# Performance work log

Hardware: AMD Instinct MI355X
Metric: run time of the kernel (lower is better)

## Reference

```python
import jax, jax.numpy as jnp
import numpy as np

N_NODES = 100000


def gcn_conv(x, W, b, src, dst, deg_inv_sqrt):
    # x: [N, Cin], W: [Cin, Cout]. PyG GCNConv: transform then normalized aggregate.
    h = x @ W  # [N, Cout]
    norm = deg_inv_sqrt[src] * deg_inv_sqrt[dst]  # [E']
    msg = h[src] * norm[:, None]  # gather + scale
    out = jax.ops.segment_sum(msg, dst, num_segments=N_NODES)
    return out + b


def setup_inputs() -> dict:
    key = jax.random.key(0)
    ks = jax.random.split(key, 8)
    C = 256
    E = 3200000
    x = jax.random.normal(ks[0], (N_NODES, C), dtype=jnp.float32)
    edge_index = jax.random.randint(ks[1], (2, E), 0, N_NODES, dtype=jnp.int64)
    s = 1.0 / np.sqrt(C)
    W1 = jax.random.uniform(ks[2], (C, C), jnp.float32, -s, s)
    b1 = jnp.zeros((C,), jnp.float32)
    W2 = jax.random.uniform(ks[3], (C, C), jnp.float32, -s, s)
    b2 = jnp.zeros((C,), jnp.float32)
    Wl = jax.random.uniform(ks[4], (C, 1), jnp.float32, -s, s)
    bl = jnp.zeros((1,), jnp.float32)
    return {"x": x, "edge_index": edge_index, "W1": W1, "b1": b1,
            "W2": W2, "b2": b2, "Wl": Wl, "bl": bl}


def reference(x, edge_index, W1, b1, W2, b2, Wl, bl):
    # add self-loops once (shared by both conv layers)
    loops = jnp.arange(N_NODES, dtype=edge_index.dtype)
    src = jnp.concatenate([edge_index[0], loops])
    dst = jnp.concatenate([edge_index[1], loops])
    # symmetric normalization: deg counts incoming edges incl. self-loops
    deg = jax.ops.segment_sum(jnp.ones_like(dst, dtype=x.dtype), dst,
                              num_segments=N_NODES)
    deg_inv_sqrt = jax.lax.rsqrt(deg)  # deg >= 1 due to self-loops
    h = jax.nn.relu(gcn_conv(x, W1, b1, src, dst, deg_inv_sqrt))
    h = jax.nn.relu(gcn_conv(h, W2, b2, src, dst, deg_inv_sqrt))
    return h @ Wl + bl  # [N, 1]
```

## Files before the change

kernel.cpp:

```cpp
#include <hip/hip_runtime.h>

#define NN 100000
#define CC 256
#define EE 3200000

typedef __attribute__((ext_vector_type(8))) short bf16x8;
typedef __attribute__((ext_vector_type(4))) float f32x4;
typedef __attribute__((ext_vector_type(4))) _Float16 f16x4;

__device__ __forceinline__ float4 f4add(float4 a, float4 b) {
  return make_float4(a.x + b.x, a.y + b.y, a.z + b.z, a.w + b.w);
}

__device__ __forceinline__ unsigned short f2bf(float f) {
  unsigned u = __float_as_uint(f);
  unsigned r = (u + 0x7fffu + ((u >> 16) & 1u)) >> 16;
  return (unsigned short)r;
}
__device__ __forceinline__ float bf2f(unsigned short h) {
  return __uint_as_float(((unsigned)h) << 16);
}

__global__ void k_deg(const int* __restrict__ dst, int* __restrict__ cnt, int n) {
  int i = blockIdx.x * blockDim.x + threadIdx.x;
  int stride = gridDim.x * blockDim.x;
  for (; i < n; i += stride) {
    unsigned d = (unsigned)dst[i];
    if (d < NN) atomicAdd(&cnt[d], 1);
  }
}

__global__ void k_dis(const int* __restrict__ cnt, float* __restrict__ dis, int n) {
  int i = blockIdx.x * blockDim.x + threadIdx.x;
  if (i < n) dis[i] = 1.0f / sqrtf((float)(cnt[i] + 1));
}

__global__ void k_scan_local(const int* __restrict__ cnt, int* __restrict__ offs,
                             int* __restrict__ bsum, int n) {
  __shared__ int wsum[16];
  int t = threadIdx.x;
  int idx = blockIdx.x * 1024 + t;
  int lane = t & 63, wv = t >> 6;
  int v = (idx < n) ? cnt[idx] : 0;
  int x = v;
#pragma unroll
  for (int d = 1; d < 64; d <<= 1) {
    int y = __shfl_up(x, d, 64);
    if (lane >= d) x += y;
  }
  if (lane == 63) wsum[wv] = x;
  __syncthreads();
  int wpre = 0, total = 0;
#pragma unroll
  for (int w = 0; w < 16; ++w) {
    int s = wsum[w];
    if (w < wv) wpre += s;
    total += s;
  }
  if (idx < n) offs[idx] = wpre + x - v;
  if (t == 0) bsum[blockIdx.x] = total;
}

__global__ void k_scan_bsum(const int* __restrict__ bsum, int* __restrict__ bbase, int nb) {
  __shared__ int wsum[2];
  int t = threadIdx.x;
  int lane = t & 63, wv = t >> 6;
  int v = (t < nb) ? bsum[t] : 0;
  int x = v;
#pragma unroll
  for (int d = 1; d < 64; d <<= 1) {
    int y = __shfl_up(x, d, 64);
    if (lane >= d) x += y;
  }
  if (lane == 63) wsum[wv] = x;
  __syncthreads();
  int pre = (wv == 1) ? wsum[0] : 0;
  if (t < nb) bbase[t] = pre + x - v;
  if (t == nb - 1) bbase[nb] = pre + x;
}

__global__ void k_scan_add(int* __restrict__ offs, const int* __restrict__ bbase,
                           int n, int nb) {
  int i = blockIdx.x * 256 + threadIdx.x;
  if (i < n) offs[i] += bbase[i >> 10];
  if (i == 0) offs[n] = bbase[nb];
}

__global__ void k_scatter(const int* __restrict__ src, const int* __restrict__ dst,
                          const int* __restrict__ offs, int* __restrict__ fill,
                          int* __restrict__ csr, int n) {
  int i = blockIdx.x * blockDim.x + threadIdx.x;
  int stride = gridDim.x * blockDim.x;
  for (; i < n; i += stride) {
    unsigned d = (unsigned)dst[i];
    unsigned s = (unsigned)src[i];
    if (d < NN && s < NN) {
      int p = offs[d] + atomicAdd(&fill[d], 1);
      csr[p] = (int)s;
    }
  }
}

__global__ void k_wsplit(const float* __restrict__ W, unsigned short* __restrict__ WTh,
                         unsigned short* __restrict__ WTl) {
  int k = blockIdx.x, n = threadIdx.x;
  float w = W[k * CC + n];
  unsigned short h = f2bf(w);
  unsigned short l = f2bf(w - bf2f(h));
  WTh[n * CC + k] = h;
  WTl[n * CC + k] = l;
}

#define LDA 40

__global__ __launch_bounds__(256) void k_gemm_mfma(
    const float* __restrict__ A, const unsigned short* __restrict__ WTh,
    const unsigned short* __restrict__ WTl, const float* __restrict__ dis,
    _Float16* __restrict__ Out, int M) {
  __shared__ unsigned short Ah[128 * LDA], Al[128 * LDA];
  __shared__ unsigned short Bh[128 * LDA], Bl[128 * LDA];
  const int tid = threadIdx.x;
  const int wave = tid >> 6, lane = tid & 63;
  const int quad = lane >> 4, l16 = lane & 15;
  const int wm = wave >> 1, wn = wave & 1;
  const int row0 = blockIdx.x * 128;
  const int n0 = blockIdx.y * 128;

  f32x4 acc[4][4];
#pragma unroll
  for (int i = 0; i < 4; ++i)
#pragma unroll
    for (int j = 0; j < 4; ++j) acc[i][j] = (f32x4){0.f, 0.f, 0.f, 0.f};

  for (int k0 = 0; k0 < CC; k0 += 32) {
#pragma unroll
    for (int q = 0; q < 4; ++q) {
      int idx = tid + 256 * q;
      int r = idx >> 3;
      int c4 = (idx & 7) << 2;
      int gr = row0 + r;
      float4 v = make_float4(0.f, 0.f, 0.f, 0.f);
      if (gr < M) v = *(const float4*)&A[(size_t)gr * CC + k0 + c4];
      ushort4 hv, lv;
      hv.x = f2bf(v.x); lv.x = f2bf(v.x - bf2f(hv.x));
      hv.y = f2bf(v.y); lv.y = f2bf(v.y - bf2f(hv.y));
      hv.z = f2bf(v.z); lv.z = f2bf(v.z - bf2f(hv.z));
      hv.w = f2bf(v.w); lv.w = f2bf(v.w - bf2f(hv.w));
      *(ushort4*)&Ah[r * LDA + c4] = hv;
      *(ushort4*)&Al[r * LDA + c4] = lv;
    }
#pragma unroll
    for (int q = 0; q < 4; ++q) {
      int idx = tid + 256 * q;
      int r = idx >> 3;
      int c4 = (idx & 7) << 2;
      const size_t g = (size_t)(n0 + r) * CC + k0 + c4;
      *(ushort4*)&Bh[r * LDA + c4] = *(const ushort4*)&WTh[g];
      *(ushort4*)&Bl[r * LDA + c4] = *(const ushort4*)&WTl[g];
    }
    __syncthreads();

    bf16x8 bh[4], bl[4];
#pragma unroll
    for (int j = 0; j < 4; ++j) {
      int br = (wn * 64 + j * 16 + l16) * LDA + quad * 8;
      bh[j] = *(const bf16x8*)&Bh[br];
      bl[j] = *(const bf16x8*)&Bl[br];
    }
#pragma unroll
    for (int i = 0; i < 4; ++i) {
      int ar = (wm * 64 + i * 16 + l16) * LDA + quad * 8;
      bf16x8 ah = *(const bf16x8*)&Ah[ar];
      bf16x8 al = *(const bf16x8*)&Al[ar];
#pragma unroll
      for (int j = 0; j < 4; ++j) {
        acc[i][j] = __builtin_amdgcn_mfma_f32_16x16x32_bf16(ah, bh[j], acc[i][j], 0, 0, 0);
        acc[i][j] = __builtin_amdgcn_mfma_f32_16x16x32_bf16(al, bh[j], acc[i][j], 0, 0, 0);
        acc[i][j] = __builtin_amdgcn_mfma_f32_16x16x32_bf16(ah, bl[j], acc[i][j], 0, 0, 0);
      }
    }
    __syncthreads();
  }

#pragma unroll
  for (int i = 0; i < 4; ++i) {
#pragma unroll
    for (int r4 = 0; r4 < 4; ++r4) {
      int r = row0 + wm * 64 + i * 16 + quad * 4 + r4;
      if (r < M) {
        float sc = dis[r];
#pragma unroll
        for (int j = 0; j < 4; ++j) {
          Out[(size_t)r * CC + n0 + wn * 64 + j * 16 + l16] =
              (_Float16)(acc[i][j][r4] * sc);
        }
      }
    }
  }
}

__global__ __launch_bounds__(256) void k_aggregate(
    const _Float16* __restrict__ hs, const int* __restrict__ offs,
    const int* __restrict__ csr, const float* __restrict__ dis,
    const float* __restrict__ bias, float* __restrict__ out, int n) {
  int node = blockIdx.x * 4 + (threadIdx.x >> 6);
  if (node >= n) return;
  int lane = threadIdx.x & 63;
  int c4 = lane << 2;
  int beg = offs[node], end = offs[node + 1];
  f16x4 sv = *(const f16x4*)&hs[(size_t)node * CC + c4];
  float4 a0 = make_float4((float)sv.x, (float)sv.y, (float)sv.z, (float)sv.w);
  float4 a1 = make_float4(0.f, 0.f, 0.f, 0.f);
  int e = beg;
  for (; e + 2 <= end; e += 2) {
    int s0 = csr[e], s1 = csr[e + 1];
    f16x4 v0 = *(const f16x4*)&hs[(size_t)s0 * CC + c4];
    f16x4 v1 = *(const f16x4*)&hs[(size_t)s1 * CC + c4];
    a0.x += (float)v0.x; a0.y += (float)v0.y; a0.z += (float)v0.z; a0.w += (float)v0.w;
    a1.x += (float)v1.x; a1.y += (float)v1.y; a1.z += (float)v1.z; a1.w += (float)v1.w;
  }
  if (e < end) {
    int s0 = csr[e];
    f16x4 v0 = *(const f16x4*)&hs[(size_t)s0 * CC + c4];
    a0.x += (float)v0.x; a0.y += (float)v0.y; a0.z += (float)v0.z; a0.w += (float)v0.w;
  }
  float4 acc = f4add(a0, a1);
  float sc = dis[node];
  float4 bv = *(const float4*)&bias[c4];
  float4 r;
  r.x = fmaxf(acc.x * sc + bv.x, 0.f);
  r.y = fmaxf(acc.y * sc + bv.y, 0.f);
  r.z = fmaxf(acc.z * sc + bv.z, 0.f);
  r.w = fmaxf(acc.w * sc + bv.w, 0.f);
  *(float4*)&out[(size_t)node * CC + c4] = r;
}

__global__ __launch_bounds__(256) void k_aggregate_final(
    const _Float16* __restrict__ hs, const int* __restrict__ offs,
    const int* __restrict__ csr, const float* __restrict__ dis,
    const float* __restrict__ bias, const float* __restrict__ Wl,
    const float* __restrict__ bl, float* __restrict__ out, int n) {
  int node = blockIdx.x * 4 + (threadIdx.x >> 6);
  if (node >= n) return;
  int lane = threadIdx.x & 63;
  int c4 = lane << 2;
  int beg = offs[node], end = offs[node + 1];
  f16x4 sv = *(const f16x4*)&hs[(size_t)node * CC + c4];
  float4 a0 = make_float4((float)sv.x, (float)sv.y, (float)sv.z, (float)sv.w);
  float4 a1 = make_float4(0.f, 0.f, 0.f, 0.f);
  int e = beg;
  for (; e + 2 <= end; e += 2) {
    int s0 = csr[e], s1 = csr[e + 1];
    f16x4 v0 = *(const f16x4*)&hs[(size_t)s0 * CC + c4];
    f16x4 v1 = *(const f16x4*)&hs[(size_t)s1 * CC + c4];
    a0.x += (float)v0.x; a0.y += (float)v0.y; a0.z += (float)v0.z; a0.w += (float)v0.w;
    a1.x += (float)v1.x; a1.y += (float)v1.y; a1.z += (float)v1.z; a1.w += (float)v1.w;
  }
  if (e < end) {
    int s0 = csr[e];
    f16x4 v0 = *(const f16x4*)&hs[(size_t)s0 * CC + c4];
    a0.x += (float)v0.x; a0.y += (float)v0.y; a0.z += (float)v0.z; a0.w += (float)v0.w;
  }
  float4 acc = f4add(a0, a1);
  float sc = dis[node];
  float4 bv = *(const float4*)&bias[c4];
  float4 w = *(const float4*)&Wl[c4];
  float s = fmaxf(acc.x * sc + bv.x, 0.f) * w.x +
            fmaxf(acc.y * sc + bv.y, 0.f) * w.y +
            fmaxf(acc.z * sc + bv.z, 0.f) * w.z +
            fmaxf(acc.w * sc + bv.w, 0.f) * w.w;
#pragma unroll
  for (int d = 32; d > 0; d >>= 1) s += __shfl_down(s, d, 64);
  if (lane == 0) out[node] = s + bl[0];
}

extern "C" void kernel_launch(void* const* d_in, const int* in_sizes, int n_in,
                              void* d_out, int out_size, void* d_ws, size_t ws_size,
                              hipStream_t stream) {
  const float* x = (const float*)d_in[0];
  const int* ei = (const int*)d_in[1];
  const float* W1 = (const float*)d_in[2];
  const float* b1 = (const float*)d_in[3];
  const float* W2 = (const float*)d_in[4];
  const float* b2 = (const float*)d_in[5];
  const float* Wl = (const float*)d_in[6];
  const float* bl = (const float*)d_in[7];
  float* out = (float*)d_out;

  const int* src = ei;
  const int* dst = ei + EE;

  char* ws = (char*)d_ws;
  size_t off = 0;
  auto alloc = [&](size_t bytes) {
    char* p = ws + off;
    off = (off + bytes + 255) & ~(size_t)255;
    return p;
  };
  float* dis = (float*)alloc((size_t)NN * 4);
  int* cnt = (int*)alloc((size_t)NN * 4);
  int* offs = (int*)alloc((size_t)(NN + 1) * 4);
  int* scanb = (int*)alloc(1024 * 4);
  int* scanb2 = (int*)alloc(1024 * 4);
  int* csr = (int*)alloc((size_t)EE * 4);
  unsigned short* W1h = (unsigned short*)alloc((size_t)CC * CC * 2);
  unsigned short* W1l = (unsigned short*)alloc((size_t)CC * CC * 2);
  unsigned short* W2h = (unsigned short*)alloc((size_t)CC * CC * 2);
  unsigned short* W2l = (unsigned short*)alloc((size_t)CC * CC * 2);
  _Float16* hsbuf = (_Float16*)alloc((size_t)NN * CC * 2);
  float* h1 = (float*)alloc((size_t)NN * CC * 4);

  hipMemsetAsync(cnt, 0, (size_t)NN * 4, stream);

  k_deg<<<2048, 256, 0, stream>>>(dst, cnt, EE);
  k_dis<<<(NN + 255) / 256, 256, 0, stream>>>(cnt, dis, NN);
  const int nb = (NN + 1023) / 1024;
  k_scan_local<<<nb, 1024, 0, stream>>>(cnt, offs, scanb, NN);
  k_scan_bsum<<<1, 128, 0, stream>>>(scanb, scanb2, nb);
  k_scan_add<<<(NN + 255) / 256, 256, 0, stream>>>(offs, scanb2, NN, nb);
  hipMemsetAsync(cnt, 0, (size_t)NN * 4, stream);
  k_scatter<<<2048, 256, 0, stream>>>(src, dst, offs, cnt, csr, EE);

  k_wsplit<<<CC, CC, 0, stream>>>(W1, W1h, W1l);
  k_wsplit<<<CC, CC, 0, stream>>>(W2, W2h, W2l);

  dim3 ggrid((NN + 127) / 128, CC / 128);
  k_gemm_mfma<<<ggrid, 256, 0, stream>>>(x, W1h, W1l, dis, hsbuf, NN);
  k_aggregate<<<(NN + 3) / 4, 256, 0, stream>>>(hsbuf, offs, csr, dis, b1, h1, NN);
  k_gemm_mfma<<<ggrid, 256, 0, stream>>>(h1, W2h, W2l, dis, hsbuf, NN);
  k_aggregate_final<<<(NN + 3) / 4, 256, 0, stream>>>(hsbuf, offs, csr, dis, b2, Wl, bl, out, NN);
}
```

Before: 1.106 ms.

## Compute full output width per GEMM block and unroll aggregation gather by four

```diff
diff --git a/kernel.cpp b/kernel.cpp
--- a/kernel.cpp
+++ b/kernel.cpp
@@ -113,18 +113,17 @@
 
 #define LDA 40
 
-__global__ __launch_bounds__(256) void k_gemm_mfma(
+__global__ __launch_bounds__(512) void k_gemm_mfma(
     const float* __restrict__ A, const unsigned short* __restrict__ WTh,
     const unsigned short* __restrict__ WTl, const float* __restrict__ dis,
     _Float16* __restrict__ Out, int M) {
   __shared__ unsigned short Ah[128 * LDA], Al[128 * LDA];
-  __shared__ unsigned short Bh[128 * LDA], Bl[128 * LDA];
+  __shared__ unsigned short Bh[256 * LDA], Bl[256 * LDA];
   const int tid = threadIdx.x;
   const int wave = tid >> 6, lane = tid & 63;
   const int quad = lane >> 4, l16 = lane & 15;
-  const int wm = wave >> 1, wn = wave & 1;
+  const int wm = wave >> 2, wn = wave & 3;
   const int row0 = blockIdx.x * 128;
-  const int n0 = blockIdx.y * 128;
 
   f32x4 acc[4][4];
 #pragma unroll
@@ -134,8 +133,8 @@
 
   for (int k0 = 0; k0 < CC; k0 += 32) {
 #pragma unroll
-    for (int q = 0; q < 4; ++q) {
-      int idx = tid + 256 * q;
+    for (int q = 0; q < 2; ++q) {
+      int idx = tid + 512 * q;
       int r = idx >> 3;
       int c4 = (idx & 7) << 2;
       int gr = row0 + r;
@@ -151,10 +150,10 @@
     }
 #pragma unroll
     for (int q = 0; q < 4; ++q) {
-      int idx = tid + 256 * q;
+      int idx = tid + 512 * q;
       int r = idx >> 3;
       int c4 = (idx & 7) << 2;
-      const size_t g = (size_t)(n0 + r) * CC + k0 + c4;
+      const size_t g = (size_t)r * CC + k0 + c4;
       *(ushort4*)&Bh[r * LDA + c4] = *(const ushort4*)&WTh[g];
       *(ushort4*)&Bl[r * LDA + c4] = *(const ushort4*)&WTl[g];
     }
@@ -191,7 +190,7 @@
         float sc = dis[r];
 #pragma unroll
         for (int j = 0; j < 4; ++j) {
-          Out[(size_t)r * CC + n0 + wn * 64 + j * 16 + l16] =
+          Out[(size_t)r * CC + wn * 64 + j * 16 + l16] =
               (_Float16)(acc[i][j][r4] * sc);
         }
       }
@@ -211,20 +210,26 @@
   f16x4 sv = *(const f16x4*)&hs[(size_t)node * CC + c4];
   float4 a0 = make_float4((float)sv.x, (float)sv.y, (float)sv.z, (float)sv.w);
   float4 a1 = make_float4(0.f, 0.f, 0.f, 0.f);
+  float4 a2 = make_float4(0.f, 0.f, 0.f, 0.f);
+  float4 a3 = make_float4(0.f, 0.f, 0.f, 0.f);
   int e = beg;
-  for (; e + 2 <= end; e += 2) {
-    int s0 = csr[e], s1 = csr[e + 1];
+  for (; e + 4 <= end; e += 4) {
+    int s0 = csr[e], s1 = csr[e + 1], s2 = csr[e + 2], s3 = csr[e + 3];
     f16x4 v0 = *(const f16x4*)&hs[(size_t)s0 * CC + c4];
     f16x4 v1 = *(const f16x4*)&hs[(size_t)s1 * CC + c4];
+    f16x4 v2 = *(const f16x4*)&hs[(size_t)s2 * CC + c4];
+    f16x4 v3 = *(const f16x4*)&hs[(size_t)s3 * CC + c4];
     a0.x += (float)v0.x; a0.y += (float)v0.y; a0.z += (float)v0.z; a0.w += (float)v0.w;
     a1.x += (float)v1.x; a1.y += (float)v1.y; a1.z += (float)v1.z; a1.w += (float)v1.w;
-  }
-  if (e < end) {
+    a2.x += (float)v2.x; a2.y += (float)v2.y; a2.z += (float)v2.z; a2.w += (float)v2.w;
+    a3.x += (float)v3.x; a3.y += (float)v3.y; a3.z += (float)v3.z; a3.w += (float)v3.w;
+  }
+  for (; e < end; ++e) {
     int s0 = csr[e];
     f16x4 v0 = *(const f16x4*)&hs[(size_t)s0 * CC + c4];
     a0.x += (float)v0.x; a0.y += (float)v0.y; a0.z += (float)v0.z; a0.w += (float)v0.w;
   }
-  float4 acc = f4add(a0, a1);
+  float4 acc = f4add(f4add(a0, a1), f4add(a2, a3));
   float sc = dis[node];
   float4 bv = *(const float4*)&bias[c4];
   float4 r;
@@ -248,20 +253,26 @@
   f16x4 sv = *(const f16x4*)&hs[(size_t)node * CC + c4];
   float4 a0 = make_float4((float)sv.x, (float)sv.y, (float)sv.z, (float)sv.w);
   float4 a1 = make_float4(0.f, 0.f, 0.f, 0.f);
+  float4 a2 = make_float4(0.f, 0.f, 0.f, 0.f);
+  float4 a3 = make_float4(0.f, 0.f, 0.f, 0.f);
   int e = beg;
-  for (; e + 2 <= end; e += 2) {
-    int s0 = csr[e], s1 = csr[e + 1];
+  for (; e + 4 <= end; e += 4) {
+    int s0 = csr[e], s1 = csr[e + 1], s2 = csr[e + 2], s3 = csr[e + 3];
     f16x4 v0 = *(const f16x4*)&hs[(size_t)s0 * CC + c4];
     f16x4 v1 = *(const f16x4*)&hs[(size_t)s1 * CC + c4];
+    f16x4 v2 = *(const f16x4*)&hs[(size_t)s2 * CC + c4];
+    f16x4 v3 = *(const f16x4*)&hs[(size_t)s3 * CC + c4];
     a0.x += (float)v0.x; a0.y += (float)v0.y; a0.z += (float)v0.z; a0.w += (float)v0.w;
     a1.x += (float)v1.x; a1.y += (float)v1.y; a1.z += (float)v1.z; a1.w += (float)v1.w;
-  }
-  if (e < end) {
+    a2.x += (float)v2.x; a2.y += (float)v2.y; a2.z += (float)v2.z; a2.w += (float)v2.w;
+    a3.x += (float)v3.x; a3.y += (float)v3.y; a3.z += (float)v3.z; a3.w += (float)v3.w;
+  }
+  for (; e < end; ++e) {
     int s0 = csr[e];
     f16x4 v0 = *(const f16x4*)&hs[(size_t)s0 * CC + c4];
     a0.x += (float)v0.x; a0.y += (float)v0.y; a0.z += (float)v0.z; a0.w += (float)v0.w;
   }
-  float4 acc = f4add(a0, a1);
+  float4 acc = f4add(f4add(a0, a1), f4add(a2, a3));
   float sc = dis[node];
   float4 bv = *(const float4*)&bias[c4];
   float4 w = *(const float4*)&Wl[c4];
@@ -324,9 +335,9 @@
   k_wsplit<<<CC, CC, 0, stream>>>(W1, W1h, W1l);
   k_wsplit<<<CC, CC, 0, stream>>>(W2, W2h, W2l);
 
-  dim3 ggrid((NN + 127) / 128, CC / 128);
-  k_gemm_mfma<<<ggrid, 256, 0, stream>>>(x, W1h, W1l, dis, hsbuf, NN);
+  const int gblocks = (NN + 127) / 128;
+  k_gemm_mfma<<<gblocks, 512, 0, stream>>>(x, W1h, W1l, dis, hsbuf, NN);
   k_aggregate<<<(NN + 3) / 4, 256, 0, stream>>>(hsbuf, offs, csr, dis, b1, h1, NN);
-  k_gemm_mfma<<<ggrid, 256, 0, stream>>>(h1, W2h, W2l, dis, hsbuf, NN);
+  k_gemm_mfma<<<gblocks, 512, 0, stream>>>(h1, W2h, W2l, dis, hsbuf, NN);
   k_aggregate_final<<<(NN + 3) / 4, 256, 0, stream>>>(hsbuf, offs, csr, dis, b2, Wl, bl, out, NN);
 }
```

Measured after the change: 1.057 ms. -4.5%, faster.
